# Optimization experiments

Measured on AMD Instinct MI355X. Metric: run time of the kernel, lower is better.

The kernel has to match this reference:

```python
import jax, jax.numpy as jnp
import numpy as np

N = 8192
F_IN = 128
F_OUT = 128
NEG_SLOPE = 0.2


def setup_inputs() -> dict:
    key = jax.random.key(0)
    k_h, k_adj, k_W, k_a = jax.random.split(key, 4)
    h = jax.random.normal(k_h, (N, F_IN), dtype=jnp.float32)
    # binary adjacency mask as float (the module multiplies scores by adj)
    adj = (jax.random.uniform(k_adj, (N, N)) < 0.05).astype(jnp.float32)
    # nn.Linear(in, out, bias=False): weight shape [out, in]
    W = jax.random.normal(k_W, (F_OUT, F_IN), dtype=jnp.float32) / np.sqrt(F_IN)
    # nn.Linear(2*out, 1, bias=False): weight shape [1, 2*out]
    a = jax.random.normal(k_a, (1, 2 * F_OUT), dtype=jnp.float32) / np.sqrt(2 * F_OUT)
    return {"h": h, "adj": adj, "W": W, "a": a}


def reference(h, adj, W, a):
    # Wh: [N, F_out]
    Wh = h @ W.T
    f = Wh.shape[-1]
    # a([Wh_i ; Wh_j]) factored: e[i, j] = leaky_relu(Wh[i]@a1 + Wh[j]@a2)
    a1 = a[0, :f]  # [F_out]
    a2 = a[0, f:]  # [F_out]
    s_i = Wh @ a1  # [N]
    s_j = Wh @ a2  # [N]
    e = jax.nn.leaky_relu(s_i[:, None] + s_j[None, :], NEG_SLOPE)  # [N, N]
    # faithful to original: softmax over dim=1 of e * adj (multiplicative mask)
    attention = jax.nn.softmax(e * adj, axis=1)  # [N, N]
    return attention @ Wh  # [N, F_out]
```

## Files before the change

kernel.cpp:

```cpp
#include <hip/hip_runtime.h>

#define N_NODES 8192
#define FDIM 128
#define NEG_SLOPE 0.2f
#define SEG 512
#define WRPB 16

__device__ __forceinline__ unsigned int f2bf(float f) {
  unsigned int u = __float_as_uint(f);
  return (u + 0x7FFFu + ((u >> 16) & 1u)) >> 16;
}

__global__ __launch_bounds__(256) void wh_fused_kernel(
    const float* __restrict__ h, const float* __restrict__ W,
    const float* __restrict__ a,
    unsigned int* __restrict__ Whb,
    float* __restrict__ s1, float* __restrict__ s2,
    float* __restrict__ S) {
  __shared__ float Wt[64 * 132];
  __shared__ float rowsLds[WRPB * 68];
  const int t = threadIdx.x;
  const int base = blockIdx.x * WRPB;
  const int g = t >> 5;
  const int c4 = (t & 31) * 4;
  float acc[2][4];
#pragma unroll
  for (int rr = 0; rr < 2; ++rr)
#pragma unroll
    for (int cc = 0; cc < 4; ++cc) acc[rr][cc] = 0.f;

#pragma unroll
  for (int h2 = 0; h2 < 2; ++h2) {
    const int k0 = h2 * 64;
    if (h2) __syncthreads();
    for (int s = 0; s < 8; ++s) {
      int idx = t + 256 * s;
      int o = idx >> 4, kq = (idx & 15) * 4;
      float4 w4 = *(const float4*)&W[o * FDIM + k0 + kq];
      Wt[(kq + 0) * 132 + o] = w4.x;
      Wt[(kq + 1) * 132 + o] = w4.y;
      Wt[(kq + 2) * 132 + o] = w4.z;
      Wt[(kq + 3) * 132 + o] = w4.w;
    }
    {
      int r = t >> 4, kq = (t & 15) * 4;
      *(float4*)&rowsLds[r * 68 + kq] =
          *(const float4*)&h[(size_t)(base + r) * FDIM + k0 + kq];
    }
    __syncthreads();
#pragma unroll 4
    for (int k = 0; k < 64; ++k) {
      float4 wv = *(const float4*)&Wt[k * 132 + c4];
      float r0 = rowsLds[(2 * g + 0) * 68 + k];
      float r1 = rowsLds[(2 * g + 1) * 68 + k];
      acc[0][0] += r0 * wv.x; acc[0][1] += r0 * wv.y;
      acc[0][2] += r0 * wv.z; acc[0][3] += r0 * wv.w;
      acc[1][0] += r1 * wv.x; acc[1][1] += r1 * wv.y;
      acc[1][2] += r1 * wv.z; acc[1][3] += r1 * wv.w;
    }
  }
#pragma unroll
  for (int rr = 0; rr < 2; ++rr) {
    int r = base + 2 * g + rr;
    unsigned int p0 = f2bf(acc[rr][0]) | (f2bf(acc[rr][1]) << 16);
    unsigned int p1 = f2bf(acc[rr][2]) | (f2bf(acc[rr][3]) << 16);
    *(uint2*)&Whb[(size_t)r * 64 + (c4 >> 1)] = make_uint2(p0, p1);
  }
  {
    float4 a1v = *(const float4*)&a[c4];
    float4 a2v = *(const float4*)&a[FDIM + c4];
#pragma unroll
    for (int rr = 0; rr < 2; ++rr) {
      float d1 = acc[rr][0] * a1v.x + acc[rr][1] * a1v.y +
                 acc[rr][2] * a1v.z + acc[rr][3] * a1v.w;
      float d2 = acc[rr][0] * a2v.x + acc[rr][1] * a2v.y +
                 acc[rr][2] * a2v.z + acc[rr][3] * a2v.w;
#pragma unroll
      for (int off = 16; off; off >>= 1) {
        d1 += __shfl_down(d1, off);
        d2 += __shfl_down(d2, off);
      }
      if ((t & 31) == 0) {
        s1[base + 2 * g + rr] = d1;
        s2[base + 2 * g + rr] = d2;
      }
    }
  }
  __syncthreads();
  float4 cs = make_float4(acc[0][0] + acc[1][0], acc[0][1] + acc[1][1],
                          acc[0][2] + acc[1][2], acc[0][3] + acc[1][3]);
  *(float4*)&rowsLds[g * FDIM + c4] = cs;
  __syncthreads();
  if (t < FDIM) {
    float s = 0.f;
#pragma unroll
    for (int gg = 0; gg < 8; ++gg) s += rowsLds[gg * FDIM + t];
    atomicAdd(&S[t], s);
  }
}

__device__ __forceinline__ float4 ntload4(const float4* p) {
  typedef float f4v __attribute__((ext_vector_type(4)));
  f4v v = __builtin_nontemporal_load((const f4v*)p);
  return make_float4(v[0], v[1], v[2], v[3]);
}

__device__ __forceinline__ int mbcnt64(unsigned long long b) {
  return (int)__builtin_amdgcn_mbcnt_hi(
      (unsigned)(b >> 32), __builtin_amdgcn_mbcnt_lo((unsigned)b, 0u));
}

__global__ __launch_bounds__(256, 8) void gat_row_kernel(
    const float* __restrict__ adj, const unsigned int* __restrict__ Whb,
    const float* __restrict__ s1, const float* __restrict__ s2,
    const float* __restrict__ S, float* __restrict__ out) {
  const int i = blockIdx.x;
  const int t = threadIdx.x;
  const int lane = t & 63;
  const int wave = t >> 6;
  __shared__ float2 pairs[4 * SEG];
  __shared__ int counts[4];
  __shared__ float red[4];
  __shared__ float red2[4];
  __shared__ float fpart[4][FDIM];

  const float s1i = s1[i];
  const float4* __restrict__ arow = (const float4*)(adj + (size_t)i * N_NODES);
  float2* __restrict__ mypairs = pairs + wave * SEG;

  int cbase = 0;
#pragma unroll
  for (int half8 = 0; half8 < 2; ++half8) {
    float4 av[4];
#pragma unroll
    for (int it = 0; it < 4; ++it)
      av[it] = ntload4(&arow[(half8 * 4 + it) * 256 + t]);
#pragma unroll
    for (int it = 0; it < 4; ++it) {
      const int j4 = (half8 * 4 + it) * 256 + t;
      float v[4] = {av[it].x, av[it].y, av[it].z, av[it].w};
#pragma unroll
      for (int c = 0; c < 4; ++c) {
        bool pred = (v[c] != 0.f);
        unsigned long long b = __ballot(pred);
        if (pred) {
          int pos = cbase + mbcnt64(b);
          if (pos < SEG) ((int*)&mypairs[pos])[1] = j4 * 4 + c;
        }
        cbase += (int)__popcll(b);
      }
    }
  }
  const int mycnt = cbase < SEG ? cbase : SEG;
  if (lane == 0) counts[wave] = mycnt;

  float lmax = -1e30f;
  for (int k = lane; k < mycnt; k += 64) {
    int j = ((const int*)&mypairs[k])[1];
    float e = s1i + s2[j];
    e = e > 0.f ? e : NEG_SLOPE * e;
    mypairs[k].x = e;
    lmax = fmaxf(lmax, e);
  }
  for (int off = 32; off; off >>= 1) lmax = fmaxf(lmax, __shfl_down(lmax, off));
  if (lane == 0) red[wave] = lmax;
  __syncthreads();
  const int cnt = counts[0] + counts[1] + counts[2] + counts[3];
  float m = fmaxf(fmaxf(red[0], red[1]), fmaxf(red[2], red[3]));
  if (cnt < N_NODES) m = fmaxf(m, 0.f);
  const float em = __expf(-m);

  float lsum = 0.f;
  for (int k = lane; k < mycnt; k += 64) {
    float p = __expf(mypairs[k].x - m);
    mypairs[k].x = p;
    lsum += p;
  }
  for (int off = 32; off; off >>= 1) lsum += __shfl_down(lsum, off);
  if (lane == 0) red2[wave] = lsum;

  const int half = lane >> 5, lq = lane & 31;
  const uint2* __restrict__ Whb2 = (const uint2*)Whb;
  float ax = 0.f, ay = 0.f, az = 0.f, aw = 0.f;
  const int nit = (mycnt + 1) >> 1;
  int it = 0;
  for (; it + 3 < nit; it += 4) {
#pragma unroll
    for (int c = 0; c < 4; ++c) {
      int p = 2 * (it + c) + half;
      bool ok = p < mycnt;
      float2 pr = mypairs[ok ? p : 0];
      int j = ((const int*)&pr)[1];
      uint2 d = Whb2[((size_t)j << 5) + lq];
      float w = ok ? pr.x - em : 0.f;
      ax += w * __uint_as_float(d.x << 16);
      ay += w * __uint_as_float(d.x & 0xffff0000u);
      az += w * __uint_as_float(d.y << 16);
      aw += w * __uint_as_float(d.y & 0xffff0000u);
    }
  }
  for (; it < nit; ++it) {
    int p = 2 * it + half;
    bool ok = p < mycnt;
    float2 pr = mypairs[ok ? p : 0];
    int j = ((const int*)&pr)[1];
    uint2 d = Whb2[((size_t)j << 5) + lq];
    float w = ok ? pr.x - em : 0.f;
    ax += w * __uint_as_float(d.x << 16);
    ay += w * __uint_as_float(d.x & 0xffff0000u);
    az += w * __uint_as_float(d.y << 16);
    aw += w * __uint_as_float(d.y & 0xffff0000u);
  }
  ax += __shfl_down(ax, 32);
  ay += __shfl_down(ay, 32);
  az += __shfl_down(az, 32);
  aw += __shfl_down(aw, 32);
  if (lane < 32)
    *(float4*)&fpart[wave][4 * lq] = make_float4(ax, ay, az, aw);
  __syncthreads();
  if (t < FDIM) {
    float l = red2[0] + red2[1] + red2[2] + red2[3]
              + (float)(N_NODES - cnt) * em;
    float o = (fpart[0][t] + fpart[1][t] + fpart[2][t] + fpart[3][t]
               + em * S[t]) / l;
    out[(size_t)i * FDIM + t] = o;
  }
}

extern "C" void kernel_launch(void* const* d_in, const int* in_sizes, int n_in,
                              void* d_out, int out_size, void* d_ws, size_t ws_size,
                              hipStream_t stream) {
  const float* h   = (const float*)d_in[0];
  const float* adj = (const float*)d_in[1];
  const float* W   = (const float*)d_in[2];
  const float* a   = (const float*)d_in[3];
  float* out = (float*)d_out;
  unsigned int* Whb = (unsigned int*)d_ws;
  float* s1 = (float*)(Whb + (size_t)N_NODES * 64);
  float* s2 = s1 + N_NODES;
  float* S  = s2 + N_NODES;

  hipMemsetAsync(S, 0, FDIM * sizeof(float), stream);
  hipLaunchKernelGGL(wh_fused_kernel, dim3(N_NODES / WRPB), dim3(256), 0,
                     stream, h, W, a, Whb, s1, s2, S);
  hipLaunchKernelGGL(gat_row_kernel, dim3(N_NODES), dim3(256), 0, stream,
                     adj, Whb, s1, s2, S, out);
}
```

Measured before the change: 410.5 us.

## Fuse projection and attention into one persistent cooperative kernel with grid sync

Replaces the memset plus two kernel launches with a single cooperative persistent kernel. It zeroes S, computes Wh in groups of 8 rows, and processes attention rows in a grid-stride loop, with grid-wide barriers between phases. The goal is to remove launch overhead and the gaps between kernels. In exchange, occupancy is capped at 4 blocks per CU by the larger shared allocation, and the projection now uses 8 rows per block with half the threads idle while loading rows. A fallback path keeps the two-kernel launch.

```diff
diff --git a/kernel.cpp b/kernel.cpp
--- a/kernel.cpp
+++ b/kernel.cpp
@@ -1,38 +1,48 @@
 #include <hip/hip_runtime.h>
+#include <hip/hip_cooperative_groups.h>
+namespace cg = cooperative_groups;
 
 #define N_NODES 8192
 #define FDIM 128
 #define NEG_SLOPE 0.2f
 #define SEG 512
-#define WRPB 16
+#define WRPB 8
+#define WH_GROUPS (N_NODES / WRPB)
+#define LDS_FLOATS (64 * 132 + WRPB * 68)
+#define GAT_LDS (4 * SEG * 2 + 12 + 4 * FDIM)
 
 __device__ __forceinline__ unsigned int f2bf(float f) {
   unsigned int u = __float_as_uint(f);
   return (u + 0x7FFFu + ((u >> 16) & 1u)) >> 16;
 }
 
-__global__ __launch_bounds__(256) void wh_fused_kernel(
-    const float* __restrict__ h, const float* __restrict__ W,
-    const float* __restrict__ a,
-    unsigned int* __restrict__ Whb,
-    float* __restrict__ s1, float* __restrict__ s2,
-    float* __restrict__ S) {
-  __shared__ float Wt[64 * 132];
-  __shared__ float rowsLds[WRPB * 68];
+__device__ __forceinline__ float4 ntload4(const float4* p) {
+  typedef float f4v __attribute__((ext_vector_type(4)));
+  f4v v = __builtin_nontemporal_load((const f4v*)p);
+  return make_float4(v[0], v[1], v[2], v[3]);
+}
+
+__device__ __forceinline__ int mbcnt64(unsigned long long b) {
+  return (int)__builtin_amdgcn_mbcnt_hi(
+      (unsigned)(b >> 32), __builtin_amdgcn_mbcnt_lo((unsigned)b, 0u));
+}
+
+__device__ __forceinline__ void wh_group(
+    int grp, const float* __restrict__ h, const float* __restrict__ W,
+    const float* __restrict__ a, unsigned int* __restrict__ Whb,
+    float* __restrict__ s1, float* __restrict__ s2, float* __restrict__ S,
+    float* lds) {
+  float* Wt = lds;
+  float* rowsL = lds + 64 * 132;
   const int t = threadIdx.x;
-  const int base = blockIdx.x * WRPB;
+  const int base = grp * WRPB;
   const int g = t >> 5;
   const int c4 = (t & 31) * 4;
-  float acc[2][4];
-#pragma unroll
-  for (int rr = 0; rr < 2; ++rr)
-#pragma unroll
-    for (int cc = 0; cc < 4; ++cc) acc[rr][cc] = 0.f;
-
+  float acc[4] = {0.f, 0.f, 0.f, 0.f};
 #pragma unroll
   for (int h2 = 0; h2 < 2; ++h2) {
     const int k0 = h2 * 64;
-    if (h2) __syncthreads();
+    __syncthreads();
     for (int s = 0; s < 8; ++s) {
       int idx = t + 256 * s;
       int o = idx >> 4, kq = (idx & 15) * 4;
@@ -42,91 +52,63 @@
       Wt[(kq + 2) * 132 + o] = w4.z;
       Wt[(kq + 3) * 132 + o] = w4.w;
     }
-    {
+    if (t < 128) {
       int r = t >> 4, kq = (t & 15) * 4;
-      *(float4*)&rowsLds[r * 68 + kq] =
+      *(float4*)&rowsL[r * 68 + kq] =
           *(const float4*)&h[(size_t)(base + r) * FDIM + k0 + kq];
     }
     __syncthreads();
 #pragma unroll 4
     for (int k = 0; k < 64; ++k) {
       float4 wv = *(const float4*)&Wt[k * 132 + c4];
-      float r0 = rowsLds[(2 * g + 0) * 68 + k];
-      float r1 = rowsLds[(2 * g + 1) * 68 + k];
-      acc[0][0] += r0 * wv.x; acc[0][1] += r0 * wv.y;
-      acc[0][2] += r0 * wv.z; acc[0][3] += r0 * wv.w;
-      acc[1][0] += r1 * wv.x; acc[1][1] += r1 * wv.y;
-      acc[1][2] += r1 * wv.z; acc[1][3] += r1 * wv.w;
-    }
-  }
-#pragma unroll
-  for (int rr = 0; rr < 2; ++rr) {
-    int r = base + 2 * g + rr;
-    unsigned int p0 = f2bf(acc[rr][0]) | (f2bf(acc[rr][1]) << 16);
-    unsigned int p1 = f2bf(acc[rr][2]) | (f2bf(acc[rr][3]) << 16);
-    *(uint2*)&Whb[(size_t)r * 64 + (c4 >> 1)] = make_uint2(p0, p1);
-  }
+      float rv = rowsL[g * 68 + k];
+      acc[0] += rv * wv.x; acc[1] += rv * wv.y;
+      acc[2] += rv * wv.z; acc[3] += rv * wv.w;
+    }
+  }
+  const int r = base + g;
+  unsigned int p0 = f2bf(acc[0]) | (f2bf(acc[1]) << 16);
+  unsigned int p1 = f2bf(acc[2]) | (f2bf(acc[3]) << 16);
+  *(uint2*)&Whb[(size_t)r * 64 + (c4 >> 1)] = make_uint2(p0, p1);
   {
     float4 a1v = *(const float4*)&a[c4];
     float4 a2v = *(const float4*)&a[FDIM + c4];
-#pragma unroll
-    for (int rr = 0; rr < 2; ++rr) {
-      float d1 = acc[rr][0] * a1v.x + acc[rr][1] * a1v.y +
-                 acc[rr][2] * a1v.z + acc[rr][3] * a1v.w;
-      float d2 = acc[rr][0] * a2v.x + acc[rr][1] * a2v.y +
-                 acc[rr][2] * a2v.z + acc[rr][3] * a2v.w;
-#pragma unroll
-      for (int off = 16; off; off >>= 1) {
-        d1 += __shfl_down(d1, off);
-        d2 += __shfl_down(d2, off);
-      }
-      if ((t & 31) == 0) {
-        s1[base + 2 * g + rr] = d1;
-        s2[base + 2 * g + rr] = d2;
-      }
-    }
-  }
-  __syncthreads();
-  float4 cs = make_float4(acc[0][0] + acc[1][0], acc[0][1] + acc[1][1],
-                          acc[0][2] + acc[1][2], acc[0][3] + acc[1][3]);
-  *(float4*)&rowsLds[g * FDIM + c4] = cs;
+    float d1 = acc[0] * a1v.x + acc[1] * a1v.y + acc[2] * a1v.z + acc[3] * a1v.w;
+    float d2 = acc[0] * a2v.x + acc[1] * a2v.y + acc[2] * a2v.z + acc[3] * a2v.w;
+#pragma unroll
+    for (int off = 16; off; off >>= 1) {
+      d1 += __shfl_down(d1, off);
+      d2 += __shfl_down(d2, off);
+    }
+    if ((t & 31) == 0) { s1[r] = d1; s2[r] = d2; }
+  }
+  __syncthreads();
+  *(float4*)&Wt[g * FDIM + c4] = make_float4(acc[0], acc[1], acc[2], acc[3]);
   __syncthreads();
   if (t < FDIM) {
     float s = 0.f;
 #pragma unroll
-    for (int gg = 0; gg < 8; ++gg) s += rowsLds[gg * FDIM + t];
+    for (int gg = 0; gg < 8; ++gg) s += Wt[gg * FDIM + t];
     atomicAdd(&S[t], s);
   }
 }
 
-__device__ __forceinline__ float4 ntload4(const float4* p) {
-  typedef float f4v __attribute__((ext_vector_type(4)));
-  f4v v = __builtin_nontemporal_load((const f4v*)p);
-  return make_float4(v[0], v[1], v[2], v[3]);
-}
-
-__device__ __forceinline__ int mbcnt64(unsigned long long b) {
-  return (int)__builtin_amdgcn_mbcnt_hi(
-      (unsigned)(b >> 32), __builtin_amdgcn_mbcnt_lo((unsigned)b, 0u));
-}
-
-__global__ __launch_bounds__(256, 8) void gat_row_kernel(
-    const float* __restrict__ adj, const unsigned int* __restrict__ Whb,
+__device__ __forceinline__ void gat_row(
+    int i, const float* __restrict__ adj, const unsigned int* __restrict__ Whb,
     const float* __restrict__ s1, const float* __restrict__ s2,
-    const float* __restrict__ S, float* __restrict__ out) {
-  const int i = blockIdx.x;
+    const float* __restrict__ S, float* __restrict__ out, float* lds) {
   const int t = threadIdx.x;
-  const int lane = t & 63;
-  const int wave = t >> 6;
-  __shared__ float2 pairs[4 * SEG];
-  __shared__ int counts[4];
-  __shared__ float red[4];
-  __shared__ float red2[4];
-  __shared__ float fpart[4][FDIM];
-
+  const int lane = t & 63, wave = t >> 6;
+  float2* pairs = (float2*)lds;
+  int* counts = (int*)(lds + 4096);
+  float* red = lds + 4100;
+  float* red2 = lds + 4104;
+  float* fpart = lds + 4108;
+  float2* __restrict__ mypairs = pairs + wave * SEG;
+
+  __syncthreads();
   const float s1i = s1[i];
   const float4* __restrict__ arow = (const float4*)(adj + (size_t)i * N_NODES);
-  float2* __restrict__ mypairs = pairs + wave * SEG;
 
   int cbase = 0;
 #pragma unroll
@@ -142,12 +124,12 @@
 #pragma unroll
       for (int c = 0; c < 4; ++c) {
         bool pred = (v[c] != 0.f);
-        unsigned long long b = __ballot(pred);
+        unsigned long long bm = __ballot(pred);
         if (pred) {
-          int pos = cbase + mbcnt64(b);
+          int pos = cbase + mbcnt64(bm);
           if (pos < SEG) ((int*)&mypairs[pos])[1] = j4 * 4 + c;
         }
-        cbase += (int)__popcll(b);
+        cbase += (int)__popcll(bm);
       }
     }
   }
@@ -216,15 +198,49 @@
   az += __shfl_down(az, 32);
   aw += __shfl_down(aw, 32);
   if (lane < 32)
-    *(float4*)&fpart[wave][4 * lq] = make_float4(ax, ay, az, aw);
+    *(float4*)&fpart[wave * FDIM + 4 * lq] = make_float4(ax, ay, az, aw);
   __syncthreads();
   if (t < FDIM) {
     float l = red2[0] + red2[1] + red2[2] + red2[3]
               + (float)(N_NODES - cnt) * em;
-    float o = (fpart[0][t] + fpart[1][t] + fpart[2][t] + fpart[3][t]
-               + em * S[t]) / l;
+    float o = (fpart[0 * FDIM + t] + fpart[1 * FDIM + t] +
+               fpart[2 * FDIM + t] + fpart[3 * FDIM + t] + em * S[t]) / l;
     out[(size_t)i * FDIM + t] = o;
   }
+}
+
+__global__ __launch_bounds__(256, 4) void gatv2_mono_kernel(
+    const float* __restrict__ h, const float* __restrict__ adj,
+    const float* __restrict__ W, const float* __restrict__ a,
+    unsigned int* __restrict__ Whb, float* __restrict__ s1,
+    float* __restrict__ s2, float* __restrict__ S, float* __restrict__ out) {
+  cg::grid_group grid = cg::this_grid();
+  __shared__ float lds[LDS_FLOATS];
+  const int b = blockIdx.x, nb = gridDim.x;
+  if (b == 0 && threadIdx.x < FDIM) S[threadIdx.x] = 0.f;
+  grid.sync();
+  for (int grp = b; grp < WH_GROUPS; grp += nb)
+    wh_group(grp, h, W, a, Whb, s1, s2, S, lds);
+  grid.sync();
+  for (int i = b; i < N_NODES; i += nb)
+    gat_row(i, adj, Whb, s1, s2, S, out, lds);
+}
+
+__global__ __launch_bounds__(256) void wh_kernel(
+    const float* __restrict__ h, const float* __restrict__ W,
+    const float* __restrict__ a, unsigned int* __restrict__ Whb,
+    float* __restrict__ s1, float* __restrict__ s2, float* __restrict__ S) {
+  __shared__ float lds[LDS_FLOATS];
+  for (int grp = blockIdx.x; grp < WH_GROUPS; grp += gridDim.x)
+    wh_group(grp, h, W, a, Whb, s1, s2, S, lds);
+}
+
+__global__ __launch_bounds__(256, 8) void gat_kernel(
+    const float* __restrict__ adj, const unsigned int* __restrict__ Whb,
+    const float* __restrict__ s1, const float* __restrict__ s2,
+    const float* __restrict__ S, float* __restrict__ out) {
+  __shared__ float lds[GAT_LDS];
+  gat_row(blockIdx.x, adj, Whb, s1, s2, S, out, lds);
 }
 
 extern "C" void kernel_launch(void* const* d_in, const int* in_sizes, int n_in,
@@ -240,9 +256,35 @@
   float* s2 = s1 + N_NODES;
   float* S  = s2 + N_NODES;
 
+  static int coop_nblk = -2;
+  if (coop_nblk == -2) {
+    int dev = 0, coop = 0, cus = 0, mab = 0;
+    hipGetDevice(&dev);
+    hipDeviceGetAttribute(&coop, hipDeviceAttributeCooperativeLaunch, dev);
+    hipDeviceGetAttribute(&cus, hipDeviceAttributeMultiprocessorCount, dev);
+    hipError_t e = hipOccupancyMaxActiveBlocksPerMultiprocessor(
+        &mab, gatv2_mono_kernel, 256, 0);
+    if (coop && e == hipSuccess && mab >= 1 && cus >= 1) {
+      long cap = (long)mab * cus;
+      coop_nblk = (int)(cap < 1024 ? cap : 1024);
+    } else {
+      coop_nblk = -1;
+    }
+  }
+
+  if (coop_nblk > 0) {
+    void* args[] = {(void*)&h, (void*)&adj, (void*)&W, (void*)&a,
+                    (void*)&Whb, (void*)&s1, (void*)&s2, (void*)&S,
+                    (void*)&out};
+    hipError_t err = hipLaunchCooperativeKernel(
+        gatv2_mono_kernel, dim3(coop_nblk), dim3(256), args, 0u, stream);
+    if (err == hipSuccess) return;
+    coop_nblk = -1;
+  }
+
   hipMemsetAsync(S, 0, FDIM * sizeof(float), stream);
-  hipLaunchKernelGGL(wh_fused_kernel, dim3(N_NODES / WRPB), dim3(256), 0,
-                     stream, h, W, a, Whb, s1, s2, S);
-  hipLaunchKernelGGL(gat_row_kernel, dim3(N_NODES), dim3(256), 0, stream,
+  hipLaunchKernelGGL(wh_kernel, dim3(WH_GROUPS), dim3(256), 0, stream,
+                     h, W, a, Whb, s1, s2, S);
+  hipLaunchKernelGGL(gat_kernel, dim3(N_NODES), dim3(256), 0, stream,
                      adj, Whb, s1, s2, S, out);
 }
```

New measurement: 572.6 us. 39.5% more time.
